# Performance work log

Hardware: AMD Instinct MI355X
Metric: run time of the kernel (lower is better)

The kernel has to match this reference:

```python
import jax, jax.numpy as jnp
import numpy as np
import math

B, T, C, H = 4, 2048, 1024, 16
HS = C // H
EPS = 1e-5


def layernorm(x, g, b):
    mu = jnp.mean(x, axis=-1, keepdims=True)
    var = jnp.var(x, axis=-1, keepdims=True)
    return (x - mu) * jax.lax.rsqrt(var + EPS) * g + b


def setup_inputs() -> dict:
    key = jax.random.key(0)
    ks = jax.random.split(key, 7)
    rn = lambda k, s: jax.random.normal(k, s, dtype=jnp.float32) * 0.02
    return {
        "x": jax.random.normal(ks[0], (B, T, C), dtype=jnp.float32),
        "mask": jnp.tril(jnp.ones((T, T), dtype=jnp.int32)),  # causal tril buffer
        "wq": rn(ks[1], (H, HS, C)),  # stacked per-head Linear weights [out,in]
        "wk": rn(ks[2], (H, HS, C)),
        "wv": rn(ks[3], (H, HS, C)),
        "ln1_g": jnp.ones((C,), jnp.float32),
        "ln1_b": jnp.zeros((C,), jnp.float32),
        "ln2_g": jnp.ones((C,), jnp.float32),
        "ln2_b": jnp.zeros((C,), jnp.float32),
        "w1": rn(ks[4], (4 * C, C)),
        "b1": jnp.zeros((4 * C,), jnp.float32),
        "w2": rn(ks[5], (C, 4 * C)),
        "b2": jnp.zeros((C,), jnp.float32),
    }


def reference(x, mask, wq, wk, wv, ln1_g, ln1_b, ln2_g, ln2_b, w1, b1, w2, b2):
    Bx, Tx, Cx = x.shape
    h = layernorm(x, ln1_g, ln1_b)
    # per-head projections, batched over heads: [B,H,T,HS]
    q = jnp.einsum('btc,hdc->bhtd', h, wq)
    k = jnp.einsum('btc,hdc->bhtd', h, wk)
    v = jnp.einsum('btc,hdc->bhtd', h, wv)
    scores = jnp.einsum('bhtd,bhsd->bhts', q, k) * (1.0 / math.sqrt(HS))
    scores = jnp.where(mask[None, None, :Tx, :Tx] == 0, -jnp.inf, scores)
    w = jax.nn.softmax(scores, axis=-1)
    attn = jnp.einsum('bhts,bhsd->bhtd', w, v)  # [B,H,T,HS]
    attn = attn.transpose(0, 2, 1, 3).reshape(Bx, Tx, Cx)  # concat heads
    x = x + attn
    h2 = layernorm(x, ln2_g, ln2_b)
    ff = jax.nn.silu(h2 @ w1.T + b1) @ w2.T + b2  # dropout = identity (eval)
    return x + ff
```

## Files before the change

kernel.cpp:

```cpp
#include <hip/hip_runtime.h>
#include <stdint.h>

#define Bb 4
#define Tt 2048
#define Cc 1024
#define Hh 16
#define HSs 64

typedef __attribute__((ext_vector_type(8))) __bf16 bf16x8;
typedef __attribute__((ext_vector_type(4))) float f32x4;

__device__ __forceinline__ ushort f2bf(float f){
  union { float f; uint u; } c; c.f = f;
  return (ushort)((c.u + 0x8000u) >> 16);
}
__device__ __forceinline__ float bf2f(ushort u){
  union { uint u; float f; } c; c.u = ((uint)u) << 16; return c.f;
}

__device__ __forceinline__ void gload16(const void* g, void* l){
  __builtin_amdgcn_global_load_lds(
      (__attribute__((address_space(1))) void*)(g),
      (__attribute__((address_space(3))) void*)(l), 16, 0, 0);
}

__global__ __launch_bounds__(256) void cast_all_kernel(
    const float* __restrict__ wq, const float* __restrict__ wk,
    const float* __restrict__ wv, const float* __restrict__ w1,
    const float* __restrict__ w2, ushort* __restrict__ out){
  int i = (blockIdx.x * 256 + threadIdx.x) * 4;
  const float* src; int off;
  if      (i <  1048576){ src = wq; off = i; }
  else if (i <  2097152){ src = wk; off = i - 1048576; }
  else if (i <  3145728){ src = wv; off = i - 2097152; }
  else if (i <  7340032){ src = w1; off = i - 3145728; }
  else                  { src = w2; off = i - 7340032; }
  float4 v = *(const float4*)(src + off);
  ushort4 o; o.x = f2bf(v.x); o.y = f2bf(v.y); o.z = f2bf(v.z); o.w = f2bf(v.w);
  *(ushort4*)(out + i) = o;
}

__global__ __launch_bounds__(256) void add_pp_kernel(float* __restrict__ out,
    const ushort* __restrict__ p0b, const ushort* __restrict__ p1b,
    const float* __restrict__ bias){
  for (int it = 0; it < 4; ++it){
    size_t i4 = (size_t)it * 2048 * 256 + blockIdx.x * 256 + threadIdx.x;
    size_t i = i4 * 4;
    float4 o = *(const float4*)(out + i);
    ushort4 a = *(const ushort4*)(p0b + i);
    ushort4 b = *(const ushort4*)(p1b + i);
    float4 bv = *(const float4*)(bias + ((i4 & 255) * 4));
    o.x += bf2f(a.x) + bf2f(b.x) + bv.x;
    o.y += bf2f(a.y) + bf2f(b.y) + bv.y;
    o.z += bf2f(a.z) + bf2f(b.z) + bv.z;
    o.w += bf2f(a.w) + bf2f(b.w) + bv.w;
    *(float4*)(out + i) = o;
  }
}

__global__ __launch_bounds__(256) void ln1_kernel(const float* __restrict__ x,
    const float* __restrict__ gw, const float* __restrict__ bw,
    ushort* __restrict__ hout){
  int row = blockIdx.x, tid = threadIdx.x;
  size_t base = (size_t)row * Cc + tid * 4;
  float4 xv = *(const float4*)(x + base);
  float s  = xv.x + xv.y + xv.z + xv.w;
  float ss = xv.x*xv.x + xv.y*xv.y + xv.z*xv.z + xv.w*xv.w;
  #pragma unroll
  for (int off = 1; off < 64; off <<= 1){ s += __shfl_xor(s, off); ss += __shfl_xor(ss, off); }
  __shared__ float red[8];
  int wid = tid >> 6, lane = tid & 63;
  if (lane == 0){ red[wid] = s; red[4 + wid] = ss; }
  __syncthreads();
  s  = red[0] + red[1] + red[2] + red[3];
  ss = red[4] + red[5] + red[6] + red[7];
  float mu = s * (1.0f / Cc);
  float rstd = rsqrtf(ss * (1.0f / Cc) - mu * mu + 1e-5f);
  float4 gv = *(const float4*)(gw + tid * 4);
  float4 bv = *(const float4*)(bw + tid * 4);
  ushort4 o;
  o.x = f2bf((xv.x - mu) * rstd * gv.x + bv.x);
  o.y = f2bf((xv.y - mu) * rstd * gv.y + bv.y);
  o.z = f2bf((xv.z - mu) * rstd * gv.z + bv.z);
  o.w = f2bf((xv.w - mu) * rstd * gv.w + bv.w);
  *(ushort4*)(hout + base) = o;
}

__global__ __launch_bounds__(256) void ln2_kernel(const float* __restrict__ x,
    const ushort* __restrict__ attnb,
    const float* __restrict__ gw, const float* __restrict__ bw,
    float* __restrict__ x2, ushort* __restrict__ hout){
  int row = blockIdx.x, tid = threadIdx.x;
  size_t base = (size_t)row * Cc + tid * 4;
  float4 xv = *(const float4*)(x + base);
  ushort4 av = *(const ushort4*)(attnb + base);
  xv.x += bf2f(av.x); xv.y += bf2f(av.y); xv.z += bf2f(av.z); xv.w += bf2f(av.w);
  *(float4*)(x2 + base) = xv;
  float s  = xv.x + xv.y + xv.z + xv.w;
  float ss = xv.x*xv.x + xv.y*xv.y + xv.z*xv.z + xv.w*xv.w;
  #pragma unroll
  for (int off = 1; off < 64; off <<= 1){ s += __shfl_xor(s, off); ss += __shfl_xor(ss, off); }
  __shared__ float red[8];
  int wid = tid >> 6, lane = tid & 63;
  if (lane == 0){ red[wid] = s; red[4 + wid] = ss; }
  __syncthreads();
  s  = red[0] + red[1] + red[2] + red[3];
  ss = red[4] + red[5] + red[6] + red[7];
  float mu = s * (1.0f / Cc);
  float rstd = rsqrtf(ss * (1.0f / Cc) - mu * mu + 1e-5f);
  float4 gv = *(const float4*)(gw + tid * 4);
  float4 bv = *(const float4*)(bw + tid * 4);
  ushort4 o;
  o.x = f2bf((xv.x - mu) * rstd * gv.x + bv.x);
  o.y = f2bf((xv.y - mu) * rstd * gv.y + bv.y);
  o.z = f2bf((xv.z - mu) * rstd * gv.z + bv.z);
  o.w = f2bf((xv.w - mu) * rstd * gv.w + bv.w);
  *(ushort4*)(hout + base) = o;
}

#define MFMA_QUAD(AF, SI, QI, BQ) \
  { \
    _Pragma("unroll") \
    for (int mi = 0; mi < 4; ++mi){ \
      acc[(SI)*4+mi][(QI)*2+0] = __builtin_amdgcn_mfma_f32_16x16x32_bf16(AF[mi][0], BQ[0][0], acc[(SI)*4+mi][(QI)*2+0], 0,0,0); \
      acc[(SI)*4+mi][(QI)*2+0] = __builtin_amdgcn_mfma_f32_16x16x32_bf16(AF[mi][1], BQ[0][1], acc[(SI)*4+mi][(QI)*2+0], 0,0,0); \
      acc[(SI)*4+mi][(QI)*2+1] = __builtin_amdgcn_mfma_f32_16x16x32_bf16(AF[mi][0], BQ[1][0], acc[(SI)*4+mi][(QI)*2+1], 0,0,0); \
      acc[(SI)*4+mi][(QI)*2+1] = __builtin_amdgcn_mfma_f32_16x16x32_bf16(AF[mi][1], BQ[1][1], acc[(SI)*4+mi][(QI)*2+1], 0,0,0); \
    } \
  }

#define GEMM_TOP() { asm volatile("s_waitcnt lgkmcnt(0)" ::: "memory"); \
                     __builtin_amdgcn_sched_barrier(0); __builtin_amdgcn_s_setprio(1); }
#define GEMM_MID() { __builtin_amdgcn_s_setprio(0); }
#define GEMM_BAR() { __builtin_amdgcn_s_barrier(); }

template<int MODE>
__device__ __forceinline__ void gemm256_body(
    const ushort* __restrict__ A, const ushort* __restrict__ Bw,
    int N, int K, int ldO,
    ushort* __restrict__ obf, float* __restrict__ of32,
    ushort* __restrict__ p1b, const float* __restrict__ bias)
{
  __shared__ __align__(16) ushort lds[2][2][2][128 * 64];
  int tid = threadIdx.x, lane = tid & 63, wid = tid >> 6;
  int wm = wid >> 2, wn = wid & 3;
  int c = lane & 15, g = lane >> 4;
  int brow0 = (wn & 1) * 64;

  int nwg = gridDim.x, bid = blockIdx.x;
  int wgid = (bid & 7) * (nwg >> 3) + (bid >> 3);
  int m0, n0, koff = 0;
  if (MODE == 3){
    int split = wgid >> 7, rem = wgid & 127;
    m0 = (rem >> 2) << 8; n0 = (rem & 3) << 8; koff = split << 11;
  } else {
    int nTn = N >> 8;
    m0 = (wgid / nTn) << 8; n0 = (wgid % nTn) << 8;
  }

  const ushort* Ag = A  + (size_t)m0 * K + koff;
  const ushort* Bg = Bw + (size_t)n0 * K + koff;

  auto stage = [&](const ushort* gbase, int t, int ab, int hb){
    #pragma unroll
    for (int j = 0; j < 2; ++j){
      int d = j * 8192 + wid * 1024 + lane * 16;
      int row = d >> 7;
      int colb = (d & 127) ^ ((row & 7) << 4);
      gload16((const char*)gbase + ((size_t)(hb * 128 + row) * K + t * 64) * 2 + colb,
              (char*)&lds[t & 1][ab][hb][0] + j * 8192 + wid * 1024);
    }
  };

  f32x4 acc[8][4] = {};
  bf16x8 af0[4][2], af1[4][2], bq0[2][2], bq1[2][2];

  auto readA = [&](const char* Ap, int sub, bf16x8 (&af)[4][2]){
    #pragma unroll
    for (int mi = 0; mi < 4; ++mi){
      int row = sub * 64 + mi * 16 + c, sw = (row & 7) << 4;
      af[mi][0] = *(const bf16x8*)(Ap + row * 128 + ((g * 16) ^ sw));
      af[mi][1] = *(const bf16x8*)(Ap + row * 128 + ((64 + g * 16) ^ sw));
    }
  };
  auto readB = [&](const char* Bp, int hb, bf16x8 (&bq)[2][2]){
    #pragma unroll
    for (int nj = 0; nj < 2; ++nj){
      int row = brow0 + hb * 32 + nj * 16 + c, sw = (row & 7) << 4;
      bq[nj][0] = *(const bf16x8*)(Bp + row * 128 + ((g * 16) ^ sw));
      bq[nj][1] = *(const bf16x8*)(Bp + row * 128 + ((64 + g * 16) ^ sw));
    }
  };

  int nt = (MODE == 3) ? (K >> 7) : (K >> 6);

  stage(Ag, 0, 0, 0); stage(Ag, 0, 0, 1);
  stage(Bg, 0, 1, 0); stage(Bg, 0, 1, 1);
  if (nt > 1){
    stage(Bg, 1, 1, 0); stage(Bg, 1, 1, 1);
    stage(Ag, 1, 0, 0); stage(Ag, 1, 0, 1);
    asm volatile("s_waitcnt vmcnt(8)" ::: "memory");
  } else {
    asm volatile("s_waitcnt vmcnt(0)" ::: "memory");
  }
  __builtin_amdgcn_s_barrier();
  readA((const char*)&lds[0][0][wm][0], 0, af0);
  readB((const char*)&lds[0][1][wn >> 1][0], 0, bq0);

  for (int t = 0; t < nt; ++t){
    const char* Abuf  = (const char*)&lds[t & 1][0][wm][0];
    const char* Bbuf  = (const char*)&lds[t & 1][1][wn >> 1][0];
    const char* AbufN = (const char*)&lds[(t + 1) & 1][0][wm][0];
    const char* BbufN = (const char*)&lds[(t + 1) & 1][1][wn >> 1][0];

    GEMM_TOP();
    MFMA_QUAD(af0, 0, 0, bq0);
    GEMM_MID();
    readB(Bbuf, 1, bq1);
    GEMM_BAR();

    GEMM_TOP();
    MFMA_QUAD(af0, 0, 1, bq1);
    GEMM_MID();
    readA(Abuf, 1, af1);
    GEMM_BAR();

    GEMM_TOP();
    MFMA_QUAD(af1, 1, 0, bq0);
    GEMM_MID();
    if (t + 2 < nt){
      stage(Bg, t + 2, 1, 0);
      asm volatile("s_waitcnt vmcnt(2)" ::: "memory");
    } else {
      asm volatile("s_waitcnt vmcnt(0)" ::: "memory");
    }
    GEMM_BAR();

    GEMM_TOP();
    MFMA_QUAD(af1, 1, 1, bq1);
    GEMM_MID();
    if (t + 1 < nt){
      readA(AbufN, 0, af0);
      readB(BbufN, 0, bq0);
    }
    if (t + 2 < nt){
      stage(Bg, t + 2, 1, 1);
      stage(Ag, t + 2, 0, 0);
      stage(Ag, t + 2, 0, 1);
    }
    GEMM_BAR();
  }

  #pragma unroll
  for (int mi = 0; mi < 8; ++mi){
    #pragma unroll
    for (int ni = 0; ni < 4; ++ni){
      #pragma unroll
      for (int r = 0; r < 4; ++r){
        float v = acc[mi][ni][r];
        int m = m0 + wm * 128 + mi * 16 + g * 4 + r;
        int n = n0 + wn * 64 + ni * 16 + c;
        if (MODE == 0){
          int which = n >> 10;
          int nn = n & 1023;
          int b = m >> 11, t = m & (Tt - 1);
          int h = nn >> 6, d = nn & 63;
          float vv = (which == 0) ? v * 0.125f : v;
          size_t base = (size_t)which * (size_t)(Bb * Tt * Cc);
          size_t idx = (which == 2)
              ? ((((size_t)(b * Hh + h)) * HSs + d) * Tt + t)
              : ((((size_t)(b * Hh + h)) * Tt + t) * HSs + d);
          obf[base + idx] = f2bf(vv);
        } else if (MODE == 1){
          v += bias[n];
          float sv = v / (1.0f + __expf(-v));
          obf[(size_t)m * ldO + n] = f2bf(sv);
        } else {
          size_t idx = (size_t)m * N + n;
          if (koff == 0) obf[idx] = f2bf(v);
          else           p1b[idx] = f2bf(v);
        }
      }
    }
  }
}

__global__ __launch_bounds__(512, 2) void gemm_qkv_kernel(
    const ushort* __restrict__ A, const ushort* __restrict__ Bw, int N, int K,
    ushort* __restrict__ obf){
  gemm256_body<0>(A, Bw, N, K, 0, obf, nullptr, nullptr, nullptr);
}
__global__ __launch_bounds__(512, 2) void gemm_ffn1_kernel(
    const ushort* __restrict__ A, const ushort* __restrict__ Bw, int N, int K, int ldO,
    ushort* __restrict__ obf, const float* __restrict__ bias){
  gemm256_body<1>(A, Bw, N, K, ldO, obf, nullptr, nullptr, bias);
}
__global__ __launch_bounds__(512, 2) void gemm_ffn2_kernel(
    const ushort* __restrict__ A, const ushort* __restrict__ Bw, int N, int K,
    ushort* __restrict__ p0b, ushort* __restrict__ p1b){
  gemm256_body<3>(A, Bw, N, K, N, p0b, nullptr, p1b, nullptr);
}

__global__ __launch_bounds__(256, 2) void attn_kernel(
    const ushort* __restrict__ q, const ushort* __restrict__ k,
    const ushort* __restrict__ vt, ushort* __restrict__ attnb)
{
  __shared__ __align__(16) ushort Ksm[4][64 * 64];
  __shared__ __align__(16) ushort Vsm[4][64 * 64];
  __shared__ __align__(16) ushort Pl[4][32 * 64];

  int bh  = blockIdx.y;
  int p   = blockIdx.x;
  int tid = threadIdx.x, wid = tid >> 6, lane = tid & 63;
  int g = lane >> 4, c = lane & 15;
  int qbA = 15 - p, qbB = p;
  int q0A = qbA * 128 + wid * 32;
  int q0B = qbB * 128 + wid * 32;
  const ushort* Qb = q  + (size_t)bh * Tt * HSs;
  const ushort* Kb = k  + (size_t)bh * Tt * HSs;
  const ushort* Vt = vt + (size_t)bh * HSs * Tt;
  char* Pw = (char*)&Pl[wid][0];

  auto stageKV = [&](int bsel, int s0){
    #pragma unroll
    for (int hb = 0; hb < 2; ++hb){
      int i = wid + hb * 4;
      int row = i * 8 + (lane >> 3);
      int col = ((lane & 7) ^ (row & 7)) * 8;
      gload16(Kb + (size_t)(s0 + row) * HSs + col, &Ksm[bsel][i * 512]);
      gload16(Vt + (size_t)row * Tt + s0 + col,    &Vsm[bsel][i * 512]);
    }
  };

  bf16x8 qfA[2][2], qfB[2][2];
  #pragma unroll
  for (int mi = 0; mi < 2; ++mi)
    #pragma unroll
    for (int ks = 0; ks < 2; ++ks){
      qfA[mi][ks] = *(const bf16x8*)(Qb + (size_t)(q0A + mi * 16 + c) * HSs + ks * 32 + g * 8);
      qfB[mi][ks] = *(const bf16x8*)(Qb + (size_t)(q0B + mi * 16 + c) * HSs + ks * 32 + g * 8);
    }

  f32x4 oA[2][4] = {}, oB[2][4] = {};
  float lA[2][4] = {}, lB[2][4] = {};

  auto computeTile = [&](bf16x8 (&qf)[2][2], f32x4 (&o)[2][4],
                         float (&lpart)[2][4],
                         int q0w, int s0, const char* Kbuf, const char* Vbuf){
    f32x4 S[2][4] = {};
    bf16x8 kf[4][2];
    #pragma unroll
    for (int ni = 0; ni < 4; ++ni)
      #pragma unroll
      for (int ks = 0; ks < 2; ++ks)
        kf[ni][ks] = *(const bf16x8*)(Kbuf + (ni * 16 + c) * 128 + (((ks * 4 + g) ^ (c & 7)) << 4));
    __builtin_amdgcn_s_setprio(1);
    #pragma unroll
    for (int mi = 0; mi < 2; ++mi)
      #pragma unroll
      for (int ni = 0; ni < 4; ++ni)
        #pragma unroll
        for (int ks = 0; ks < 2; ++ks)
          S[mi][ni] = __builtin_amdgcn_mfma_f32_16x16x32_bf16(qf[mi][ks], kf[ni][ks], S[mi][ni], 0, 0, 0);
    __builtin_amdgcn_s_setprio(0);

    if (s0 + 63 > q0w){
      #pragma unroll
      for (int mi = 0; mi < 2; ++mi)
        #pragma unroll
        for (int ni = 0; ni < 4; ++ni)
          #pragma unroll
          for (int r = 0; r < 4; ++r){
            int tl = q0w + mi * 16 + g * 4 + r, sl = s0 + ni * 16 + c;
            if (sl > tl) S[mi][ni][r] = -1e30f;
          }
    }

    #pragma unroll
    for (int mi = 0; mi < 2; ++mi)
      #pragma unroll
      for (int r = 0; r < 4; ++r){
        int row = mi * 16 + g * 4 + r;
        float pp[4];
        #pragma unroll
        for (int ni = 0; ni < 4; ++ni){
          pp[ni] = exp2f(S[mi][ni][r] * 1.44269504f);
          *(ushort*)(Pw + row * 128 + (((ni * 32 + 2 * c) ^ ((row & 7) << 4)))) = f2bf(pp[ni]);
        }
        lpart[mi][r] += (pp[0] + pp[1]) + (pp[2] + pp[3]);
      }

    bf16x8 vf[4][2];
    #pragma unroll
    for (int dt = 0; dt < 4; ++dt)
      #pragma unroll
      for (int ks = 0; ks < 2; ++ks)
        vf[dt][ks] = *(const bf16x8*)(Vbuf + (dt * 16 + c) * 128 + (((ks * 4 + g) ^ (c & 7)) << 4));
    __builtin_amdgcn_s_setprio(1);
    #pragma unroll
    for (int mi = 0; mi < 2; ++mi){
      #pragma unroll
      for (int ks = 0; ks < 2; ++ks){
        bf16x8 pf = *(const bf16x8*)(Pw + (mi * 16 + c) * 128 + ((((ks * 4 + g) ^ (c & 7)) << 4)));
        #pragma unroll
        for (int dt = 0; dt < 4; ++dt)
          o[mi][dt] = __builtin_amdgcn_mfma_f32_16x16x32_bf16(pf, vf[dt][ks], o[mi][dt], 0, 0, 0);
      }
    }
    __builtin_amdgcn_s_setprio(0);
  };

  int nchA = 2 * qbA + 2;

  stageKV(0, 0);
  stageKV(1, 64);

  for (int ch = 0; ch < nchA; ch += 2){
    bool staged = (ch + 2 < nchA);
    if (staged){
      stageKV((ch + 2) & 3, (ch + 2) * 64);
      stageKV((ch + 3) & 3, (ch + 3) * 64);
      asm volatile("s_waitcnt vmcnt(8)" ::: "memory");
    } else {
      asm volatile("s_waitcnt vmcnt(0)" ::: "memory");
    }
    __builtin_amdgcn_sched_barrier(0);
    __builtin_amdgcn_s_barrier();

    {
      int s0 = ch * 64;
      const char* Kbuf = (const char*)&Ksm[ch & 3][0];
      const char* Vbuf = (const char*)&Vsm[ch & 3][0];
      if (s0 <= q0A + 31) computeTile(qfA, oA, lA, q0A, s0, Kbuf, Vbuf);
      if (s0 <= q0B + 31) computeTile(qfB, oB, lB, q0B, s0, Kbuf, Vbuf);
    }
    {
      int s0 = (ch + 1) * 64;
      const char* Kbuf = (const char*)&Ksm[(ch + 1) & 3][0];
      const char* Vbuf = (const char*)&Vsm[(ch + 1) & 3][0];
      if (s0 <= q0A + 31) computeTile(qfA, oA, lA, q0A, s0, Kbuf, Vbuf);
      if (s0 <= q0B + 31) computeTile(qfB, oB, lB, q0B, s0, Kbuf, Vbuf);
    }

    __builtin_amdgcn_sched_barrier(0);
    __builtin_amdgcn_s_barrier();
  }

  int b = bh >> 4, h = bh & 15;
  #pragma unroll
  for (int mi = 0; mi < 2; ++mi)
    #pragma unroll
    for (int r = 0; r < 4; ++r){
      float la = lA[mi][r];
      la += __shfl_xor(la, 1); la += __shfl_xor(la, 2);
      la += __shfl_xor(la, 4); la += __shfl_xor(la, 8);
      float lia = 1.0f / la;
      float lb = lB[mi][r];
      lb += __shfl_xor(lb, 1); lb += __shfl_xor(lb, 2);
      lb += __shfl_xor(lb, 4); lb += __shfl_xor(lb, 8);
      float lib = 1.0f / lb;
      #pragma unroll
      for (int dt = 0; dt < 4; ++dt){
        int tA = q0A + mi * 16 + g * 4 + r;
        int tB = q0B + mi * 16 + g * 4 + r;
        attnb[((size_t)(b * Tt + tA)) * Cc + h * HSs + dt * 16 + c] = f2bf(oA[mi][dt][r] * lia);
        attnb[((size_t)(b * Tt + tB)) * Cc + h * HSs + dt * 16 + c] = f2bf(oB[mi][dt][r] * lib);
      }
    }
}

extern "C" void kernel_launch(void* const* d_in, const int* in_sizes, int n_in,
                              void* d_out, int out_size, void* d_ws, size_t ws_size,
                              hipStream_t stream) {
  (void)in_sizes; (void)n_in; (void)out_size; (void)ws_size;
  const float* x    = (const float*)d_in[0];
  const float* wq   = (const float*)d_in[2];
  const float* wk   = (const float*)d_in[3];
  const float* wv   = (const float*)d_in[4];
  const float* ln1g = (const float*)d_in[5];
  const float* ln1b = (const float*)d_in[6];
  const float* ln2g = (const float*)d_in[7];
  const float* ln2b = (const float*)d_in[8];
  const float* w1   = (const float*)d_in[9];
  const float* b1   = (const float*)d_in[10];
  const float* w2   = (const float*)d_in[11];
  const float* b2   = (const float*)d_in[12];
  float* out = (float*)d_out;

  char* ws = (char*)d_ws;
  const size_t SZ_ACT = (size_t)Bb * Tt * Cc * 2;
  ushort* h1    = (ushort*)(ws);
  ushort* qbuf  = (ushort*)(ws + SZ_ACT);
  ushort* kbuf  = (ushort*)(ws + 2 * SZ_ACT);
  ushort* vbuf  = (ushort*)(ws + 3 * SZ_ACT);
  ushort* attnb = (ushort*)(ws + 4 * SZ_ACT);
  ushort* h2    = (ushort*)(ws + 5 * SZ_ACT);
  ushort* h3    = (ushort*)(ws + 6 * SZ_ACT);
  ushort* p0b   = (ushort*)(ws + SZ_ACT);
  ushort* p1b   = (ushort*)(ws + 2 * SZ_ACT);
  char*   wsw   = ws + 6 * SZ_ACT + (size_t)Bb * Tt * 4 * Cc * 2;
  ushort* wqb = (ushort*)(wsw);
  ushort* w1b = (ushort*)(wsw + 3 * (size_t)Cc * Cc * 2);
  ushort* w2b = (ushort*)(wsw + 3 * (size_t)Cc * Cc * 2 + (size_t)4 * Cc * Cc * 2);

  cast_all_kernel<<<dim3(11264), 256, 0, stream>>>(wq, wk, wv, w1, w2, wqb);

  ln1_kernel<<<dim3(Bb * Tt), 256, 0, stream>>>(x, ln1g, ln1b, h1);

  gemm_qkv_kernel<<<dim3(32 * 12), 512, 0, stream>>>(h1, wqb, 3 * Cc, Cc, qbuf);

  attn_kernel<<<dim3(8, Bb * Hh), 256, 0, stream>>>(qbuf, kbuf, vbuf, attnb);

  ln2_kernel<<<dim3(Bb * Tt), 256, 0, stream>>>(x, attnb, ln2g, ln2b, out, h2);

  gemm_ffn1_kernel<<<dim3(32 * 16), 512, 0, stream>>>(h2, w1b, 4 * Cc, Cc, 4 * Cc, h3, b1);
  gemm_ffn2_kernel<<<dim3(256), 512, 0, stream>>>(h3, w2b, Cc, 4 * Cc, p0b, p1b);
  add_pp_kernel<<<dim3(2048), 256, 0, stream>>>(out, p0b, p1b, b2);
}
```

Before: 362.6 us.

## Use dedicated 128x128-tile GEMM for FFN1 and fold log2e into Q scale

```diff
diff --git a/kernel.cpp b/kernel.cpp
--- a/kernel.cpp
+++ b/kernel.cpp
@@ -265,16 +265,12 @@
           int nn = n & 1023;
           int b = m >> 11, t = m & (Tt - 1);
           int h = nn >> 6, d = nn & 63;
-          float vv = (which == 0) ? v * 0.125f : v;
+          float vv = (which == 0) ? v * 0.18033688f : v;
           size_t base = (size_t)which * (size_t)(Bb * Tt * Cc);
           size_t idx = (which == 2)
               ? ((((size_t)(b * Hh + h)) * HSs + d) * Tt + t)
               : ((((size_t)(b * Hh + h)) * Tt + t) * HSs + d);
           obf[base + idx] = f2bf(vv);
-        } else if (MODE == 1){
-          v += bias[n];
-          float sv = v / (1.0f + __expf(-v));
-          obf[(size_t)m * ldO + n] = f2bf(sv);
         } else {
           size_t idx = (size_t)m * N + n;
           if (koff == 0) obf[idx] = f2bf(v);
@@ -290,15 +286,94 @@
     ushort* __restrict__ obf){
   gemm256_body<0>(A, Bw, N, K, 0, obf, nullptr, nullptr, nullptr);
 }
-__global__ __launch_bounds__(512, 2) void gemm_ffn1_kernel(
-    const ushort* __restrict__ A, const ushort* __restrict__ Bw, int N, int K, int ldO,
-    ushort* __restrict__ obf, const float* __restrict__ bias){
-  gemm256_body<1>(A, Bw, N, K, ldO, obf, nullptr, nullptr, bias);
-}
 __global__ __launch_bounds__(512, 2) void gemm_ffn2_kernel(
     const ushort* __restrict__ A, const ushort* __restrict__ Bw, int N, int K,
     ushort* __restrict__ p0b, ushort* __restrict__ p1b){
   gemm256_body<3>(A, Bw, N, K, N, p0b, nullptr, p1b, nullptr);
+}
+
+__global__ __launch_bounds__(256, 2) void gemm128_ffn1_kernel(
+    const ushort* __restrict__ A, const ushort* __restrict__ Bw,
+    int N, int K, int ldO,
+    ushort* __restrict__ obf, const float* __restrict__ bias)
+{
+  __shared__ __align__(16) ushort lds[2][2][128 * 64];
+  int tid = threadIdx.x, lane = tid & 63, wid = tid >> 6;
+  int wm = wid >> 1, wn = wid & 1;
+  int c = lane & 15, g = lane >> 4;
+
+  int nwg = gridDim.x, bid = blockIdx.x;
+  int wgid = (bid & 7) * (nwg >> 3) + (bid >> 3);
+  int nTn = N >> 7;
+  int m0 = (wgid / nTn) << 7, n0 = (wgid % nTn) << 7;
+
+  const ushort* Ag = A  + (size_t)m0 * K;
+  const ushort* Bg = Bw + (size_t)n0 * K;
+
+  auto stage = [&](int t, int bsel){
+    #pragma unroll
+    for (int j = 0; j < 4; ++j){
+      int d = j * 4096 + wid * 1024 + lane * 16;
+      int row = d >> 7;
+      int colb = (d & 127) ^ ((row & 7) << 4);
+      gload16((const char*)Ag + ((size_t)row * K + t * 64) * 2 + colb,
+              (char*)&lds[bsel][0][0] + j * 4096 + wid * 1024);
+      gload16((const char*)Bg + ((size_t)row * K + t * 64) * 2 + colb,
+              (char*)&lds[bsel][1][0] + j * 4096 + wid * 1024);
+    }
+  };
+
+  f32x4 acc[4][4] = {};
+  int nt = K >> 6;
+
+  stage(0, 0);
+  asm volatile("s_waitcnt vmcnt(0)" ::: "memory");
+  __builtin_amdgcn_s_barrier();
+
+  for (int t = 0; t < nt; ++t){
+    int buf = t & 1;
+    if (t + 1 < nt) stage(t + 1, buf ^ 1);
+
+    const char* Ap = (const char*)&lds[buf][0][0];
+    const char* Bp = (const char*)&lds[buf][1][0];
+    #pragma unroll
+    for (int ks = 0; ks < 2; ++ks){
+      bf16x8 af[4], bq[4];
+      #pragma unroll
+      for (int i = 0; i < 4; ++i){
+        int ra = wm * 64 + i * 16 + c;
+        af[i] = *(const bf16x8*)(Ap + ra * 128 + ((ks * 64 + g * 16) ^ ((ra & 7) << 4)));
+        int rb = wn * 64 + i * 16 + c;
+        bq[i] = *(const bf16x8*)(Bp + rb * 128 + ((ks * 64 + g * 16) ^ ((rb & 7) << 4)));
+      }
+      asm volatile("s_waitcnt lgkmcnt(0)" ::: "memory");
+      __builtin_amdgcn_sched_barrier(0);
+      __builtin_amdgcn_s_setprio(1);
+      #pragma unroll
+      for (int mi = 0; mi < 4; ++mi)
+        #pragma unroll
+        for (int ni = 0; ni < 4; ++ni)
+          acc[mi][ni] = __builtin_amdgcn_mfma_f32_16x16x32_bf16(af[mi], bq[ni], acc[mi][ni], 0, 0, 0);
+      __builtin_amdgcn_s_setprio(0);
+    }
+
+    if (t + 1 < nt) asm volatile("s_waitcnt vmcnt(0)" ::: "memory");
+    __builtin_amdgcn_sched_barrier(0);
+    __builtin_amdgcn_s_barrier();
+  }
+
+  #pragma unroll
+  for (int mi = 0; mi < 4; ++mi)
+    #pragma unroll
+    for (int ni = 0; ni < 4; ++ni)
+      #pragma unroll
+      for (int r = 0; r < 4; ++r){
+        int m = m0 + wm * 64 + mi * 16 + g * 4 + r;
+        int n = n0 + wn * 64 + ni * 16 + c;
+        float v = acc[mi][ni][r] + bias[n];
+        float sv = v / (1.0f + __expf(-v));
+        obf[(size_t)m * ldO + n] = f2bf(sv);
+      }
 }
 
 __global__ __launch_bounds__(256, 2) void attn_kernel(
@@ -384,7 +459,7 @@
         float pp[4];
         #pragma unroll
         for (int ni = 0; ni < 4; ++ni){
-          pp[ni] = exp2f(S[mi][ni][r] * 1.44269504f);
+          pp[ni] = exp2f(S[mi][ni][r]);
           *(ushort*)(Pw + row * 128 + (((ni * 32 + 2 * c) ^ ((row & 7) << 4)))) = f2bf(pp[ni]);
         }
         lpart[mi][r] += (pp[0] + pp[1]) + (pp[2] + pp[3]);
@@ -513,7 +588,7 @@
 
   ln2_kernel<<<dim3(Bb * Tt), 256, 0, stream>>>(x, attnb, ln2g, ln2b, out, h2);
 
-  gemm_ffn1_kernel<<<dim3(32 * 16), 512, 0, stream>>>(h2, w1b, 4 * Cc, Cc, 4 * Cc, h3, b1);
+  gemm128_ffn1_kernel<<<dim3(2048), 256, 0, stream>>>(h2, w1b, 4 * Cc, Cc, 4 * Cc, h3, b1);
   gemm_ffn2_kernel<<<dim3(256), 512, 0, stream>>>(h3, w2b, Cc, 4 * Cc, p0b, p1b);
   add_pp_kernel<<<dim3(2048), 256, 0, stream>>>(out, p0b, p1b, b2);
 }
```

Result: slower. 373.9 us (+3.1%).
